# Kernel tuning notes

Hardware: AMD Instinct MI355X
Metric: run time of the kernel (lower is better)

Reference implementation:

```python
import jax, jax.numpy as jnp
import numpy as np

N = 50000
E = 800000
IN_C, HID_C, OUT_C = 128, 256, 128
BN_EPS = 1e-5


def glorot(key, shape):
    fan_in, fan_out = shape
    lim = float(np.sqrt(6.0 / (fan_in + fan_out)))
    return jax.random.uniform(key, shape, jnp.float32, -lim, lim)


def setup_inputs() -> dict:
    key = jax.random.key(0)
    ks = jax.random.split(key, 16)
    inp = {
        "x": jax.random.normal(ks[0], (N, IN_C), jnp.float32),
        "edge_index": jax.random.randint(ks[1], (2, E), 0, N, jnp.int64),
        # SAGEConv 1 (in->hid): lin_l has bias, lin_r has no bias (PyG default)
        "wl1": glorot(ks[2], (IN_C, HID_C)), "bl1": jnp.zeros((HID_C,), jnp.float32),
        "wr1": glorot(ks[3], (IN_C, HID_C)),
        # SAGEConv 2 (hid->hid)
        "wl2": glorot(ks[4], (HID_C, HID_C)), "bl2": jnp.zeros((HID_C,), jnp.float32),
        "wr2": glorot(ks[5], (HID_C, HID_C)),
        # SAGEConv 3 (hid->out)
        "wl3": glorot(ks[6], (HID_C, OUT_C)), "bl3": jnp.zeros((OUT_C,), jnp.float32),
        "wr3": glorot(ks[7], (HID_C, OUT_C)),
        # BatchNorm params (eval mode: running stats)
        "bn1_w": jnp.ones((HID_C,), jnp.float32), "bn1_b": jnp.zeros((HID_C,), jnp.float32),
        "bn1_m": jax.random.normal(ks[8], (HID_C,), jnp.float32) * 0.1,
        "bn1_v": jax.random.uniform(ks[9], (HID_C,), jnp.float32, 0.5, 1.5),
        "bn2_w": jnp.ones((HID_C,), jnp.float32), "bn2_b": jnp.zeros((HID_C,), jnp.float32),
        "bn2_m": jax.random.normal(ks[10], (HID_C,), jnp.float32) * 0.1,
        "bn2_v": jax.random.uniform(ks[11], (HID_C,), jnp.float32, 0.5, 1.5),
    }
    return inp


def sage_conv(x, src, dst, wl, bl, wr):
    # mean aggregation of source-node features at destination nodes
    agg = jax.ops.segment_sum(x[src], dst, num_segments=N)          # [N, d_in]
    deg = jax.ops.segment_sum(jnp.ones((E,), x.dtype), dst, num_segments=N)
    mean = agg / jnp.maximum(deg, 1.0)[:, None]
    return mean @ wl + bl + x @ wr                                   # [N, d_out]


def batch_norm(x, w, b, m, v):
    return (x - m) * jax.lax.rsqrt(v + BN_EPS) * w + b


def reference(x, edge_index, wl1, bl1, wr1, wl2, bl2, wr2, wl3, bl3, wr3,
              bn1_w, bn1_b, bn1_m, bn1_v, bn2_w, bn2_b, bn2_m, bn2_v):
    src, dst = edge_index[0], edge_index[1]
    # layer 1: SAGEConv -> BN -> ReLU (dropout is identity in eval mode)
    h = sage_conv(x, src, dst, wl1, bl1, wr1)
    h = jax.nn.relu(batch_norm(h, bn1_w, bn1_b, bn1_m, bn1_v))
    # layer 2
    h = sage_conv(h, src, dst, wl2, bl2, wr2)
    h = jax.nn.relu(batch_norm(h, bn2_w, bn2_b, bn2_m, bn2_v))
    # output layer: plain SAGEConv
    return sage_conv(h, src, dst, wl3, bl3, wr3)
```

## Files before the change

kernel.cpp:

```cpp
#include <hip/hip_runtime.h>
#include <hip/hip_bf16.h>

#define NN 50000
#define NE 800000
#define NSB 49
#define AGG_BLOCKS 2048

typedef __attribute__((ext_vector_type(8))) short bh8;
typedef __attribute__((ext_vector_type(4))) float f32x4;

static __device__ __forceinline__ unsigned short f2bf(float f){
  unsigned u = __float_as_uint(f);
  unsigned r = (u + 0x7fffu + ((u >> 16) & 1u)) >> 16;
  return (unsigned short)r;
}
static __device__ __forceinline__ float bflo(unsigned u){ return __uint_as_float(u << 16); }
static __device__ __forceinline__ float bfhi(unsigned u){ return __uint_as_float(u & 0xffff0000u); }
static __device__ __forceinline__ unsigned packbf2(float lo, float hi){
  return ((unsigned)f2bf(hi) << 16) | (unsigned)f2bf(lo);
}
static __device__ __forceinline__ unsigned char f2fp8(float v){
  return (unsigned char)(__builtin_amdgcn_cvt_pk_fp8_f32(v, v, 0, false) & 0xff);
}

static __device__ __forceinline__ void gload16(const void* g, void* l){
  __builtin_amdgcn_global_load_lds(
      (const __attribute__((address_space(1))) unsigned int*)g,
      (__attribute__((address_space(3))) unsigned int*)l, 16, 0, 0);
}

__global__ void hist_k(const int* __restrict__ dstv, int* __restrict__ cnt,
                       int* __restrict__ rank){
  int i = blockIdx.x * 256 + threadIdx.x;
  if (i < NE) rank[i] = atomicAdd(&cnt[dstv[i]], 1);
}

__global__ __launch_bounds__(256) void scan1_k(const int* __restrict__ cnt,
                                               int* __restrict__ rowp,
                                               int* __restrict__ bsum){
  __shared__ int sa[256], sb[256];
  const int t = threadIdx.x, blk = blockIdx.x;
  const int base = blk * 1024 + t * 4;
  int4 v = make_int4(0, 0, 0, 0);
  if (base + 3 < NN) v = *reinterpret_cast<const int4*>(cnt + base);
  else if (base < NN){
    v.x = cnt[base];
    if (base + 1 < NN) v.y = cnt[base + 1];
    if (base + 2 < NN) v.z = cnt[base + 2];
  }
  const int s = v.x + v.y + v.z + v.w;
  sa[t] = s; __syncthreads();
  int* a = sa; int* b = sb;
  for (int off = 1; off < 256; off <<= 1){
    int val = a[t]; if (t >= off) val += a[t - off];
    b[t] = val; __syncthreads();
    int* tmp = a; a = b; b = tmp;
  }
  const int ex = a[t] - s;
  if (base < NN){
    rowp[base] = ex;
    if (base + 1 < NN) rowp[base + 1] = ex + v.x;
    if (base + 2 < NN) rowp[base + 2] = ex + v.x + v.y;
    if (base + 3 < NN) rowp[base + 3] = ex + v.x + v.y + v.z;
  }
  if (t == 255) bsum[blk] = a[255];
}

__global__ void scan2_k(int* __restrict__ bsum){
  __shared__ int s[64];
  const int t = threadIdx.x;
  s[t] = (t < NSB) ? bsum[t] : 0;
  __syncthreads();
  if (t == 0){
    int run = 0;
    for (int i = 0; i < NSB; ++i){ int c = s[i]; s[i] = run; run += c; }
  }
  __syncthreads();
  if (t < NSB) bsum[t] = s[t];
}

__global__ __launch_bounds__(256) void scan3_k(int* __restrict__ rowp,
                                               const int* __restrict__ bsum){
  const int blk = blockIdx.x;
  const int base = blk * 1024 + threadIdx.x * 4;
  const int off = bsum[blk];
  #pragma unroll
  for (int i = 0; i < 4; ++i){
    int idx = base + i;
    if (idx < NN) rowp[idx] += off;
  }
  if (blk == 0 && threadIdx.x == 0) rowp[NN] = NE;
}

__global__ __launch_bounds__(256) void fill_k(const int* __restrict__ srcv,
                       const int* __restrict__ dstv,
                       const int* __restrict__ rank,
                       const int* __restrict__ rowp, int* __restrict__ csrc){
  const int part  = blockIdx.x & 7;
  const int chunk = blockIdx.x >> 3;
  const int lo = part * (NN / 8);
  const int hi = lo + (NN / 8);
  const int base = chunk * (NE / 128);
  const int endi = base + (NE / 128);
  for (int i = base + threadIdx.x; i < endi; i += 256){
    int d = dstv[i];
    if (d >= lo && d < hi){
      csrc[rowp[d] + rank[i]] = srcv[i];
    }
  }
}

__global__ void f2b_k(const float4* __restrict__ x, uint2* __restrict__ xb,
                      unsigned* __restrict__ xq){
  int i = blockIdx.x * 256 + threadIdx.x;
  if (i < NN * 128 / 4){
    float4 v = x[i];
    uint2 o; o.x = packbf2(v.x, v.y); o.y = packbf2(v.z, v.w);
    xb[i] = o;
    int w = 0;
    w = __builtin_amdgcn_cvt_pk_fp8_f32(v.x, v.y, w, false);
    w = __builtin_amdgcn_cvt_pk_fp8_f32(v.z, v.w, w, true);
    xq[i] = (unsigned)w;
  }
}

__global__ void prep_k(const float* __restrict__ wl1, const float* __restrict__ wr1,
                       const float* __restrict__ wl2, const float* __restrict__ wr2,
                       const float* __restrict__ wl3, const float* __restrict__ wr3,
                       const float* __restrict__ bl1, const float* __restrict__ bl2,
                       const float* __restrict__ bn1w, const float* __restrict__ bn1b,
                       const float* __restrict__ bn1m, const float* __restrict__ bn1v,
                       const float* __restrict__ bn2w, const float* __restrict__ bn2b,
                       const float* __restrict__ bn2m, const float* __restrict__ bn2v,
                       unsigned short* __restrict__ B1t, unsigned short* __restrict__ B2t,
                       unsigned short* __restrict__ B3t,
                       float* __restrict__ S1, float* __restrict__ T1,
                       float* __restrict__ S2, float* __restrict__ T2){
  int i = blockIdx.x * 256 + threadIdx.x;
  if (i < 65536){
    int n = i >> 8, k = i & 255;
    float v = (k < 128) ? wl1[k * 256 + n] : wr1[(k - 128) * 256 + n];
    B1t[n * 256 + k] = f2bf(v);
  } else if (i < 65536 + 131072){
    int j = i - 65536; int n = j >> 9, k = j & 511;
    float v = (k < 256) ? wl2[k * 256 + n] : wr2[(k - 256) * 256 + n];
    B2t[n * 512 + k] = f2bf(v);
  } else if (i < 65536 + 131072 + 65536){
    int j = i - (65536 + 131072); int n = j >> 8, k = j & 255;
    float v = (n < 128) ? wl3[k * 128 + n] : wr3[k * 128 + (n - 128)];
    B3t[n * 256 + k] = f2bf(v);
  } else if (i < 65536 + 131072 + 65536 + 512){
    int j = i - (65536 + 131072 + 65536);
    if (j < 256){
      float s = bn1w[j] * rsqrtf(bn1v[j] + 1e-5f);
      S1[j] = s; T1[j] = (bl1[j] - bn1m[j]) * s + bn1b[j];
    } else {
      int c = j - 256;
      float s = bn2w[c] * rsqrtf(bn2v[c] + 1e-5f);
      S2[c] = s; T2[c] = (bl2[c] - bn2m[c]) * s + bn2b[c];
    }
  }
}

__global__ __launch_bounds__(256) void agg128q_k(const unsigned short* __restrict__ featq,
                         unsigned* __restrict__ out,
                         const int* __restrict__ rowp, const int* __restrict__ csrc){
  const int lane = threadIdx.x & 63;
  const int node0 = __builtin_amdgcn_readfirstlane(blockIdx.x * 4 + (threadIdx.x >> 6));
  const int nw = gridDim.x * 4;
  for (int node = node0; node < NN; node += nw){
    const int start = rowp[node], end = rowp[node + 1];
    float a0 = 0.f, a1 = 0.f, b0 = 0.f, b1 = 0.f;
    int e = start;
    for (; e + 7 < end; e += 8){
      unsigned u0 = featq[(size_t)csrc[e]     * 64 + lane];
      unsigned u1 = featq[(size_t)csrc[e + 1] * 64 + lane];
      unsigned u2 = featq[(size_t)csrc[e + 2] * 64 + lane];
      unsigned u3 = featq[(size_t)csrc[e + 3] * 64 + lane];
      unsigned u4 = featq[(size_t)csrc[e + 4] * 64 + lane];
      unsigned u5 = featq[(size_t)csrc[e + 5] * 64 + lane];
      unsigned u6 = featq[(size_t)csrc[e + 6] * 64 + lane];
      unsigned u7 = featq[(size_t)csrc[e + 7] * 64 + lane];
      a0 += __builtin_amdgcn_cvt_f32_fp8(u0, 0); a1 += __builtin_amdgcn_cvt_f32_fp8(u0, 1);
      b0 += __builtin_amdgcn_cvt_f32_fp8(u1, 0); b1 += __builtin_amdgcn_cvt_f32_fp8(u1, 1);
      a0 += __builtin_amdgcn_cvt_f32_fp8(u2, 0); a1 += __builtin_amdgcn_cvt_f32_fp8(u2, 1);
      b0 += __builtin_amdgcn_cvt_f32_fp8(u3, 0); b1 += __builtin_amdgcn_cvt_f32_fp8(u3, 1);
      a0 += __builtin_amdgcn_cvt_f32_fp8(u4, 0); a1 += __builtin_amdgcn_cvt_f32_fp8(u4, 1);
      b0 += __builtin_amdgcn_cvt_f32_fp8(u5, 0); b1 += __builtin_amdgcn_cvt_f32_fp8(u5, 1);
      a0 += __builtin_amdgcn_cvt_f32_fp8(u6, 0); a1 += __builtin_amdgcn_cvt_f32_fp8(u6, 1);
      b0 += __builtin_amdgcn_cvt_f32_fp8(u7, 0); b1 += __builtin_amdgcn_cvt_f32_fp8(u7, 1);
    }
    for (; e < end; ++e){
      unsigned u = featq[(size_t)csrc[e] * 64 + lane];
      a0 += __builtin_amdgcn_cvt_f32_fp8(u, 0); a1 += __builtin_amdgcn_cvt_f32_fp8(u, 1);
    }
    int d = end - start;
    float inv = 1.f / (float)(d > 0 ? d : 1);
    out[(size_t)node * 64 + lane] = packbf2((a0 + b0) * inv, (a1 + b1) * inv);
  }
}

#define DEC8(u, x0, x1, x2, x3) { \
  x0 += __builtin_amdgcn_cvt_f32_fp8((u), 0); \
  x1 += __builtin_amdgcn_cvt_f32_fp8((u), 1); \
  x2 += __builtin_amdgcn_cvt_f32_fp8((u), 2); \
  x3 += __builtin_amdgcn_cvt_f32_fp8((u), 3); }

__global__ __launch_bounds__(256) void agg256q_k(const unsigned* __restrict__ featq, unsigned* __restrict__ out,
                         const int* __restrict__ rowp, const int* __restrict__ csrc){
  const int lane = threadIdx.x & 63;
  const int node0 = __builtin_amdgcn_readfirstlane(blockIdx.x * 4 + (threadIdx.x >> 6));
  const int nw = gridDim.x * 4;
  for (int node = node0; node < NN; node += nw){
    const int start = rowp[node], end = rowp[node + 1];
    float a0 = 0.f, a1 = 0.f, a2 = 0.f, a3 = 0.f;
    float b0 = 0.f, b1 = 0.f, b2 = 0.f, b3 = 0.f;
    int e = start;
    for (; e + 7 < end; e += 8){
      unsigned u0 = featq[(size_t)csrc[e]     * 64 + lane];
      unsigned u1 = featq[(size_t)csrc[e + 1] * 64 + lane];
      unsigned u2 = featq[(size_t)csrc[e + 2] * 64 + lane];
      unsigned u3 = featq[(size_t)csrc[e + 3] * 64 + lane];
      unsigned u4 = featq[(size_t)csrc[e + 4] * 64 + lane];
      unsigned u5 = featq[(size_t)csrc[e + 5] * 64 + lane];
      unsigned u6 = featq[(size_t)csrc[e + 6] * 64 + lane];
      unsigned u7 = featq[(size_t)csrc[e + 7] * 64 + lane];
      DEC8(u0, a0, a1, a2, a3) DEC8(u1, b0, b1, b2, b3)
      DEC8(u2, a0, a1, a2, a3) DEC8(u3, b0, b1, b2, b3)
      DEC8(u4, a0, a1, a2, a3) DEC8(u5, b0, b1, b2, b3)
      DEC8(u6, a0, a1, a2, a3) DEC8(u7, b0, b1, b2, b3)
    }
    for (; e < end; ++e){
      unsigned u = featq[(size_t)csrc[e] * 64 + lane];
      DEC8(u, a0, a1, a2, a3)
    }
    int d = end - start;
    float inv = 1.f / (float)(d > 0 ? d : 1);
    uint2 o; o.x = packbf2((a0 + b0) * inv, (a1 + b1) * inv);
    o.y = packbf2((a2 + b2) * inv, (a3 + b3) * inv);
    *reinterpret_cast<uint2*>(out + (size_t)node * 128 + lane * 2) = o;
  }
}

__global__ __launch_bounds__(256) void final_k(const unsigned short* __restrict__ tq, float* __restrict__ out,
                        const int* __restrict__ rowp, const int* __restrict__ csrc,
                        const float* __restrict__ bl3){
  const int lane = threadIdx.x & 63;
  const int node0 = __builtin_amdgcn_readfirstlane(blockIdx.x * 4 + (threadIdx.x >> 6));
  const int nw = gridDim.x * 4;
  for (int node = node0; node < NN; node += nw){
    const int start = rowp[node], end = rowp[node + 1];
    float a0 = 0.f, a1 = 0.f, b0 = 0.f, b1 = 0.f;
    int e = start;
    for (; e + 7 < end; e += 8){
      unsigned u0 = tq[(size_t)csrc[e]     * 64 + lane];
      unsigned u1 = tq[(size_t)csrc[e + 1] * 64 + lane];
      unsigned u2 = tq[(size_t)csrc[e + 2] * 64 + lane];
      unsigned u3 = tq[(size_t)csrc[e + 3] * 64 + lane];
      unsigned u4 = tq[(size_t)csrc[e + 4] * 64 + lane];
      unsigned u5 = tq[(size_t)csrc[e + 5] * 64 + lane];
      unsigned u6 = tq[(size_t)csrc[e + 6] * 64 + lane];
      unsigned u7 = tq[(size_t)csrc[e + 7] * 64 + lane];
      a0 += __builtin_amdgcn_cvt_f32_fp8(u0, 0); a1 += __builtin_amdgcn_cvt_f32_fp8(u0, 1);
      b0 += __builtin_amdgcn_cvt_f32_fp8(u1, 0); b1 += __builtin_amdgcn_cvt_f32_fp8(u1, 1);
      a0 += __builtin_amdgcn_cvt_f32_fp8(u2, 0); a1 += __builtin_amdgcn_cvt_f32_fp8(u2, 1);
      b0 += __builtin_amdgcn_cvt_f32_fp8(u3, 0); b1 += __builtin_amdgcn_cvt_f32_fp8(u3, 1);
      a0 += __builtin_amdgcn_cvt_f32_fp8(u4, 0); a1 += __builtin_amdgcn_cvt_f32_fp8(u4, 1);
      b0 += __builtin_amdgcn_cvt_f32_fp8(u5, 0); b1 += __builtin_amdgcn_cvt_f32_fp8(u5, 1);
      a0 += __builtin_amdgcn_cvt_f32_fp8(u6, 0); a1 += __builtin_amdgcn_cvt_f32_fp8(u6, 1);
      b0 += __builtin_amdgcn_cvt_f32_fp8(u7, 0); b1 += __builtin_amdgcn_cvt_f32_fp8(u7, 1);
    }
    for (; e < end; ++e){
      unsigned u = tq[(size_t)csrc[e] * 64 + lane];
      a0 += __builtin_amdgcn_cvt_f32_fp8(u, 0); a1 += __builtin_amdgcn_cvt_f32_fp8(u, 1);
    }
    int d = end - start;
    float inv = 1.f / (float)(d > 0 ? d : 1);
    float2* o = reinterpret_cast<float2*>(out + (size_t)node * 128) + lane;
    float2 v = *o;
    v.x += (a0 + b0) * inv + bl3[lane * 2];
    v.y += (a1 + b1) * inv + bl3[lane * 2 + 1];
    *o = v;
  }
}

template<int KTOT, int K0, int MODE>
__global__ __launch_bounds__(256) void gemm_k(
    const unsigned short* __restrict__ A0, const unsigned short* __restrict__ A1,
    const unsigned short* __restrict__ Bt,
    const float* __restrict__ S, const float* __restrict__ Tt,
    unsigned short* __restrict__ outB, unsigned char* __restrict__ outQ,
    float* __restrict__ outF, int M)
{
  __shared__ __align__(16) unsigned char lds[49152];
  const int tid = threadIdx.x;
  const int lane = tid & 63;
  const int wv = tid >> 6;
  const int wm = wv >> 1, wn = wv & 1;

  const int nwg = gridDim.x;
  const int q = nwg >> 3, r8 = nwg & 7;
  const int xcd = blockIdx.x & 7, idx = blockIdx.x >> 3;
  const int wg = (xcd < r8) ? xcd * (q + 1) + idx : r8 * (q + 1) + (xcd - r8) * q + idx;
  const int bm = wg >> 1, bn = wg & 1;

  const int rr0 = tid >> 2,         g0 = (tid & 3) ^ ((tid >> 3) & 3);
  const int rr1 = (tid + 256) >> 2, g1 = ((tid + 256) & 3) ^ (((tid + 256) >> 3) & 3);
  int growA0 = bm * 128 + rr0; if (growA0 > M - 1) growA0 = M - 1;
  int growA1 = bm * 128 + rr1; if (growA1 > M - 1) growA1 = M - 1;
  const size_t browA0 = (size_t)(bn * 128 + rr0) * KTOT;
  const size_t browA1 = (size_t)(bn * 128 + rr1) * KTOT;

  const int l15 = lane & 15, kg = lane >> 4;
  const int slot = (kg ^ ((l15 >> 1) & 3)) * 16;

  constexpr int NT = KTOT / 32;

  auto STAGE = [&](int buf, int kt){
    const int kb = kt * 32;
    const unsigned short* Ap; int pitch, kk;
    if (KTOT == K0 || kb < K0){ Ap = A0; pitch = K0; kk = kb; }
    else { Ap = A1; pitch = KTOT - K0; kk = kb - K0; }
    unsigned char* base = lds + buf * 16384;
    gload16(Ap + (size_t)growA0 * pitch + kk + g0 * 8, base + tid * 16);
    gload16(Ap + (size_t)growA1 * pitch + kk + g1 * 8, base + 4096 + tid * 16);
    gload16(Bt + browA0 + kb + g0 * 8, base + 8192 + tid * 16);
    gload16(Bt + browA1 + kb + g1 * 8, base + 12288 + tid * 16);
  };

  f32x4 acc[4][4];
  #pragma unroll
  for (int i = 0; i < 4; ++i)
    #pragma unroll
    for (int j = 0; j < 4; ++j){ acc[i][j][0]=0.f; acc[i][j][1]=0.f; acc[i][j][2]=0.f; acc[i][j][3]=0.f; }

  STAGE(0, 0);
  if (NT > 1) STAGE(1, 1);

  int rb = 0, sb = 2;
  for (int kt = 0; kt < NT; ++kt){
    if (kt < NT - 1) asm volatile("s_waitcnt vmcnt(4)" ::: "memory");
    else             asm volatile("s_waitcnt vmcnt(0)" ::: "memory");
    __builtin_amdgcn_s_barrier();
    __builtin_amdgcn_sched_barrier(0);

    if (kt + 2 < NT){ STAGE(sb, kt + 2); sb = (sb == 2) ? 0 : sb + 1; }

    unsigned char* base = lds + rb * 16384;
    rb = (rb == 2) ? 0 : rb + 1;

    bh8 af[4], bf[4];
    #pragma unroll
    for (int mi = 0; mi < 4; ++mi){
      int rA = wm * 64 + mi * 16 + l15;
      af[mi] = *reinterpret_cast<const bh8*>(base + rA * 64 + slot);
    }
    #pragma unroll
    for (int ni = 0; ni < 4; ++ni){
      int rB = wn * 64 + ni * 16 + l15;
      bf[ni] = *reinterpret_cast<const bh8*>(base + 8192 + rB * 64 + slot);
    }
    __builtin_amdgcn_s_setprio(1);
    #pragma unroll
    for (int mi = 0; mi < 4; ++mi)
      #pragma unroll
      for (int ni = 0; ni < 4; ++ni)
        acc[mi][ni] = __builtin_amdgcn_mfma_f32_16x16x32_bf16(af[mi], bf[ni], acc[mi][ni], 0, 0, 0);
    __builtin_amdgcn_s_setprio(0);
  }

  #pragma unroll
  for (int mi = 0; mi < 4; ++mi){
    int rbase = bm * 128 + wm * 64 + mi * 16 + ((lane >> 4) << 2);
    #pragma unroll
    for (int ni = 0; ni < 4; ++ni){
      int col = bn * 128 + wn * 64 + ni * 16 + (lane & 15);
      #pragma unroll
      for (int j = 0; j < 4; ++j){
        int row = rbase + j;
        if (row < M){
          float v = acc[mi][ni][j];
          if (MODE == 0){
            v = v * S[col] + Tt[col];
            v = v > 0.f ? v : 0.f;
            outB[(size_t)row * 256 + col] = f2bf(v);
            if (outQ) outQ[(size_t)row * 256 + col] = f2fp8(v);
          } else {
            if (col < 128) outQ[(size_t)row * 128 + col] = f2fp8(v);
            else           outF[(size_t)row * 128 + (col - 128)] = v;
          }
        }
      }
    }
  }
}

extern "C" void kernel_launch(void* const* d_in, const int* in_sizes, int n_in,
                              void* d_out, int out_size, void* d_ws, size_t ws_size,
                              hipStream_t stream) {
  (void)in_sizes; (void)n_in; (void)out_size; (void)ws_size;
  const float* x   = (const float*)d_in[0];
  const int*   ei  = (const int*)d_in[1];
  const int*   srcv = ei;
  const int*   dstv = ei + NE;
  const float* wl1 = (const float*)d_in[2];
  const float* bl1 = (const float*)d_in[3];
  const float* wr1 = (const float*)d_in[4];
  const float* wl2 = (const float*)d_in[5];
  const float* bl2 = (const float*)d_in[6];
  const float* wr2 = (const float*)d_in[7];
  const float* wl3 = (const float*)d_in[8];
  const float* bl3 = (const float*)d_in[9];
  const float* wr3 = (const float*)d_in[10];
  const float* bn1w = (const float*)d_in[11];
  const float* bn1b = (const float*)d_in[12];
  const float* bn1m = (const float*)d_in[13];
  const float* bn1v = (const float*)d_in[14];
  const float* bn2w = (const float*)d_in[15];
  const float* bn2b = (const float*)d_in[16];
  const float* bn2m = (const float*)d_in[17];
  const float* bn2v = (const float*)d_in[18];

  char* ws = (char*)d_ws;
  size_t off = 0;
  auto alloc = [&](size_t bytes) -> void* {
    void* p = ws + off;
    off += (bytes + 255) & ~(size_t)255;
    return p;
  };
  int* cnt  = (int*)alloc((size_t)NN * 4);
  int* rank = (int*)alloc((size_t)NE * 4);
  int* rowp = (int*)alloc((size_t)(NN + 1) * 4);
  int* csrc = (int*)alloc((size_t)NE * 4);
  int* bsum = (int*)alloc((size_t)NSB * 4);
  unsigned short* B1t = (unsigned short*)alloc(256 * 256 * 2);
  unsigned short* B2t = (unsigned short*)alloc(256 * 512 * 2);
  unsigned short* B3t = (unsigned short*)alloc(256 * 256 * 2);
  float* S1 = (float*)alloc(256 * 4);
  float* T1 = (float*)alloc(256 * 4);
  float* S2 = (float*)alloc(256 * 4);
  float* T2 = (float*)alloc(256 * 4);
  unsigned short* xb   = (unsigned short*)alloc((size_t)NN * 128 * 2);
  unsigned short* agg1 = (unsigned short*)alloc((size_t)NN * 128 * 2);
  unsigned short* h1   = (unsigned short*)alloc((size_t)NN * 256 * 2);
  unsigned short* h2   = (unsigned short*)alloc((size_t)NN * 256 * 2);
  unsigned short* agg2 = xb;
  unsigned char*  h1q  = (unsigned char*)h2;
  unsigned*       xq   = (unsigned*)((unsigned char*)h2 + (size_t)NN * 256);
  unsigned char*  tq   = (unsigned char*)h1;
  float* outp = (float*)d_out;

  hipMemsetAsync(cnt, 0, (size_t)NN * 4, stream);
  hist_k<<<(NE + 255) / 256, 256, 0, stream>>>(dstv, cnt, rank);
  scan1_k<<<NSB, 256, 0, stream>>>(cnt, rowp, bsum);
  scan2_k<<<1, 64, 0, stream>>>(bsum);
  scan3_k<<<NSB, 256, 0, stream>>>(rowp, bsum);
  fill_k<<<1024, 256, 0, stream>>>(srcv, dstv, rank, rowp, csrc);
  prep_k<<<1026, 256, 0, stream>>>(wl1, wr1, wl2, wr2, wl3, wr3, bl1, bl2,
                                   bn1w, bn1b, bn1m, bn1v, bn2w, bn2b, bn2m, bn2v,
                                   B1t, B2t, B3t, S1, T1, S2, T2);
  f2b_k<<<(NN * 128 / 4 + 255) / 256, 256, 0, stream>>>((const float4*)x, (uint2*)xb, xq);

  agg128q_k<<<AGG_BLOCKS, 256, 0, stream>>>((const unsigned short*)xq, (unsigned*)agg1, rowp, csrc);
  gemm_k<256, 128, 0><<<782, 256, 0, stream>>>(agg1, xb, B1t, S1, T1, h1, h1q, nullptr, NN);
  agg256q_k<<<AGG_BLOCKS, 256, 0, stream>>>((const unsigned*)h1q, (unsigned*)agg2, rowp, csrc);
  gemm_k<512, 256, 0><<<782, 256, 0, stream>>>(agg2, h1, B2t, S2, T2, h2, nullptr, nullptr, NN);
  gemm_k<256, 256, 1><<<782, 256, 0, stream>>>(h2, h2, B3t, nullptr, nullptr, nullptr, tq, outp, NN);
  final_k<<<AGG_BLOCKS, 256, 0, stream>>>((const unsigned short*)tq, outp, rowp, csrc, bl3);
}
```

Baseline: 252.3 us.

## Restructure GEMM into barrier-free per-wave private tiles with smaller blocks

Each GEMM workgroup now has two waves. Each wave owns a private double-buffered LDS region and loads its own A and B tiles, so the block-wide s_barrier is gone. The block tile shrinks from 128x256 to 64x256, which doubles the grid, and each wave duplicates the A-tile loads its partner also makes. This removes cross-wave synchronisation stalls and lowers LDS per block for higher occupancy, at the cost of redundant global and LDS traffic for A and one less pipeline stage.

```diff
diff --git a/kernel.cpp b/kernel.cpp
--- a/kernel.cpp
+++ b/kernel.cpp
@@ -285,34 +285,36 @@
 }
 
 template<int KTOT, int K0, int MODE>
-__global__ __launch_bounds__(256) void gemm_k(
+__global__ __launch_bounds__(128) void gemm_k(
     const unsigned short* __restrict__ A0, const unsigned short* __restrict__ A1,
     const unsigned short* __restrict__ Bt,
     const float* __restrict__ S, const float* __restrict__ Tt,
     unsigned short* __restrict__ outB, unsigned char* __restrict__ outQ,
     float* __restrict__ outF, int M)
 {
-  __shared__ __align__(16) unsigned char lds[49152];
+  __shared__ __align__(16) unsigned char lds[32768];
   const int tid = threadIdx.x;
   const int lane = tid & 63;
   const int wv = tid >> 6;
-  const int wm = wv >> 1, wn = wv & 1;
-
   const int nwg = gridDim.x;
   const int q = nwg >> 3, r8 = nwg & 7;
   const int xcd = blockIdx.x & 7, idx = blockIdx.x >> 3;
   const int wg = (xcd < r8) ? xcd * (q + 1) + idx : r8 * (q + 1) + (xcd - r8) * q + idx;
   const int bm = wg >> 1, bn = wg & 1;
 
-  const int rr0 = tid >> 2,         g0 = (tid & 3) ^ ((tid >> 3) & 3);
-  const int rr1 = (tid + 256) >> 2, g1 = ((tid + 256) & 3) ^ (((tid + 256) >> 3) & 3);
-  int growA0 = bm * 128 + rr0; if (growA0 > M - 1) growA0 = M - 1;
-  int growA1 = bm * 128 + rr1; if (growA1 > M - 1) growA1 = M - 1;
-  const size_t browA0 = (size_t)(bn * 128 + rr0) * KTOT;
-  const size_t browA1 = (size_t)(bn * 128 + rr1) * KTOT;
-
   const int l15 = lane & 15, kg = lane >> 4;
   const int slot = (kg ^ ((l15 >> 1) & 3)) * 16;
+  const int g   = (lane & 3) ^ ((lane >> 3) & 3);
+  const int r16 = lane >> 2;
+
+  const int ncol0 = bn * 128 + wv * 64;
+  int arow[4];
+  #pragma unroll
+  for (int i = 0; i < 4; ++i){
+    int r = bm * 64 + i * 16 + r16;
+    arow[i] = (r > M - 1) ? (M - 1) : r;
+  }
+  unsigned char* wbase = lds + wv * 16384;
 
   constexpr int NT = KTOT / 32;
 
@@ -321,11 +323,14 @@
     const unsigned short* Ap; int pitch, kk;
     if (KTOT == K0 || kb < K0){ Ap = A0; pitch = K0; kk = kb; }
     else { Ap = A1; pitch = KTOT - K0; kk = kb - K0; }
-    unsigned char* base = lds + buf * 16384;
-    gload16(Ap + (size_t)growA0 * pitch + kk + g0 * 8, base + tid * 16);
-    gload16(Ap + (size_t)growA1 * pitch + kk + g1 * 8, base + 4096 + tid * 16);
-    gload16(Bt + browA0 + kb + g0 * 8, base + 8192 + tid * 16);
-    gload16(Bt + browA1 + kb + g1 * 8, base + 12288 + tid * 16);
+    unsigned char* base = wbase + buf * 8192;
+    #pragma unroll
+    for (int i = 0; i < 4; ++i)
+      gload16(Ap + (size_t)arow[i] * pitch + kk + g * 8, base + i * 1024 + lane * 16);
+    #pragma unroll
+    for (int i = 0; i < 4; ++i)
+      gload16(Bt + (size_t)(ncol0 + i * 16 + r16) * KTOT + kb + g * 8,
+              base + 4096 + i * 1024 + lane * 16);
   };
 
   f32x4 acc[4][4];
@@ -337,29 +342,24 @@
   STAGE(0, 0);
   if (NT > 1) STAGE(1, 1);
 
-  int rb = 0, sb = 2;
   for (int kt = 0; kt < NT; ++kt){
-    if (kt < NT - 1) asm volatile("s_waitcnt vmcnt(4)" ::: "memory");
+    if (kt < NT - 1) asm volatile("s_waitcnt vmcnt(8)" ::: "memory");
     else             asm volatile("s_waitcnt vmcnt(0)" ::: "memory");
-    __builtin_amdgcn_s_barrier();
     __builtin_amdgcn_sched_barrier(0);
 
-    if (kt + 2 < NT){ STAGE(sb, kt + 2); sb = (sb == 2) ? 0 : sb + 1; }
-
-    unsigned char* base = lds + rb * 16384;
-    rb = (rb == 2) ? 0 : rb + 1;
-
+    unsigned char* base = wbase + (kt & 1) * 8192;
     bh8 af[4], bf[4];
     #pragma unroll
-    for (int mi = 0; mi < 4; ++mi){
-      int rA = wm * 64 + mi * 16 + l15;
-      af[mi] = *reinterpret_cast<const bh8*>(base + rA * 64 + slot);
-    }
-    #pragma unroll
-    for (int ni = 0; ni < 4; ++ni){
-      int rB = wn * 64 + ni * 16 + l15;
-      bf[ni] = *reinterpret_cast<const bh8*>(base + 8192 + rB * 64 + slot);
-    }
+    for (int mi = 0; mi < 4; ++mi)
+      af[mi] = *reinterpret_cast<const bh8*>(base + (mi * 16 + l15) * 64 + slot);
+    #pragma unroll
+    for (int ni = 0; ni < 4; ++ni)
+      bf[ni] = *reinterpret_cast<const bh8*>(base + 4096 + (ni * 16 + l15) * 64 + slot);
+
+    asm volatile("s_waitcnt lgkmcnt(0)" ::: "memory");
+    __builtin_amdgcn_sched_barrier(0);
+    if (kt + 2 < NT) STAGE(kt & 1, kt + 2);
+
     __builtin_amdgcn_s_setprio(1);
     #pragma unroll
     for (int mi = 0; mi < 4; ++mi)
@@ -371,10 +371,10 @@
 
   #pragma unroll
   for (int mi = 0; mi < 4; ++mi){
-    int rbase = bm * 128 + wm * 64 + mi * 16 + ((lane >> 4) << 2);
+    int rbase = bm * 64 + mi * 16 + (kg << 2);
     #pragma unroll
     for (int ni = 0; ni < 4; ++ni){
-      int col = bn * 128 + wn * 64 + ni * 16 + (lane & 15);
+      int col = ncol0 + ni * 16 + l15;
       #pragma unroll
       for (int j = 0; j < 4; ++j){
         int row = rbase + j;
@@ -462,9 +462,9 @@
   f2b_k<<<(NN * 128 / 4 + 255) / 256, 256, 0, stream>>>((const float4*)x, (uint2*)xb, xq);
 
   agg128q_k<<<AGG_BLOCKS, 256, 0, stream>>>((const unsigned short*)xq, (unsigned*)agg1, rowp, csrc);
-  gemm_k<256, 128, 0><<<782, 256, 0, stream>>>(agg1, xb, B1t, S1, T1, h1, h1q, nullptr, NN);
+  gemm_k<256, 128, 0><<<1564, 128, 0, stream>>>(agg1, xb, B1t, S1, T1, h1, h1q, nullptr, NN);
   agg256q_k<<<AGG_BLOCKS, 256, 0, stream>>>((const unsigned*)h1q, (unsigned*)agg2, rowp, csrc);
-  gemm_k<512, 256, 0><<<782, 256, 0, stream>>>(agg2, h1, B2t, S2, T2, h2, nullptr, nullptr, NN);
-  gemm_k<256, 256, 1><<<782, 256, 0, stream>>>(h2, h2, B3t, nullptr, nullptr, nullptr, tq, outp, NN);
+  gemm_k<512, 256, 0><<<1564, 128, 0, stream>>>(agg2, h1, B2t, S2, T2, h2, nullptr, nullptr, NN);
+  gemm_k<256, 256, 1><<<1564, 128, 0, stream>>>(h2, h2, B3t, nullptr, nullptr, nullptr, tq, outp, NN);
   final_k<<<AGG_BLOCKS, 256, 0, stream>>>((const unsigned short*)tq, outp, rowp, csrc, bl3);
 }
```

Result: slower. 268.3 us (+6.3%).

## Fuse layer-2 GEMM with layer-3 projection GEMM via LDS-resident hidden tile

Applied to the files above, without the earlier changes.

Merges the layer-2 SAGE GEMM (with BN+ReLU epilogue) and the layer-3 projection GEMM into one kernel. The 64x256 bf16 h2 tile stays in LDS, swizzled, and feeds the second MFMA loop directly, so h2 is never written to or re-read from global memory and one launch is removed. The second loop reads B3 straight from global memory with no LDS staging, and the larger LDS footprint plus two accumulator sets may reduce occupancy. tq is moved to alias h2's buffer.

```diff
diff --git a/kernel.cpp b/kernel.cpp
--- a/kernel.cpp
+++ b/kernel.cpp
@@ -395,6 +395,147 @@
   }
 }
 
+__global__ __launch_bounds__(256) void gemm23_k(
+    const unsigned short* __restrict__ A0 ,
+    const unsigned short* __restrict__ A1 ,
+    const unsigned short* __restrict__ B2 ,
+    const unsigned short* __restrict__ B3 ,
+    const float* __restrict__ S, const float* __restrict__ Tt,
+    unsigned char* __restrict__ tq, float* __restrict__ outF, int M)
+{
+  __shared__ __align__(16) unsigned char lds[61440];
+  const int tid = threadIdx.x;
+  const int lane = tid & 63;
+  const int wv = tid >> 6;
+
+  const int nwg = gridDim.x;
+  const int q = nwg >> 3, r8 = nwg & 7;
+  const int xcd = blockIdx.x & 7, idx = blockIdx.x >> 3;
+  const int bm = (xcd < r8) ? xcd * (q + 1) + idx : r8 * (q + 1) + (xcd - r8) * q + idx;
+
+  const int l15 = lane & 15, kg = lane >> 4;
+  const int slot = (kg ^ ((l15 >> 1) & 3)) * 16;
+  const int rr = tid >> 2;
+  const int g  = (tid & 3) ^ ((tid >> 3) & 3);
+  int grow = bm * 64 + rr; if (grow > M - 1) grow = M - 1;
+
+  auto STAGE = [&](int buf, int kt){
+    const int kb = kt * 32;
+    const unsigned short* Ap = (kb < 256) ? A0 : A1;
+    const int kk = (kb < 256) ? kb : kb - 256;
+    unsigned char* base = lds + buf * 20480;
+    gload16(Ap + (size_t)grow * 256 + kk + g * 8, base + tid * 16);
+    gload16(B2 + (size_t)(rr      ) * 512 + kb + g * 8, base +  4096 + tid * 16);
+    gload16(B2 + (size_t)(rr +  64) * 512 + kb + g * 8, base +  8192 + tid * 16);
+    gload16(B2 + (size_t)(rr + 128) * 512 + kb + g * 8, base + 12288 + tid * 16);
+    gload16(B2 + (size_t)(rr + 192) * 512 + kb + g * 8, base + 16384 + tid * 16);
+  };
+
+  f32x4 acc[4][4];
+  #pragma unroll
+  for (int i = 0; i < 4; ++i)
+    #pragma unroll
+    for (int j = 0; j < 4; ++j){ acc[i][j][0]=0.f; acc[i][j][1]=0.f; acc[i][j][2]=0.f; acc[i][j][3]=0.f; }
+
+  STAGE(0, 0);
+  STAGE(1, 1);
+
+  int rb = 0, sb = 2;
+  #pragma unroll 1
+  for (int kt = 0; kt < 16; ++kt){
+    if (kt < 15) asm volatile("s_waitcnt vmcnt(5)" ::: "memory");
+    else         asm volatile("s_waitcnt vmcnt(0)" ::: "memory");
+    __builtin_amdgcn_s_barrier();
+    __builtin_amdgcn_sched_barrier(0);
+
+    if (kt + 2 < 16){ STAGE(sb, kt + 2); sb = (sb == 2) ? 0 : sb + 1; }
+
+    unsigned char* base = lds + rb * 20480;
+    rb = (rb == 2) ? 0 : rb + 1;
+
+    bh8 af[4], bf[4];
+    #pragma unroll
+    for (int mi = 0; mi < 4; ++mi)
+      af[mi] = *reinterpret_cast<const bh8*>(base + (mi * 16 + l15) * 64 + slot);
+    #pragma unroll
+    for (int ni = 0; ni < 4; ++ni)
+      bf[ni] = *reinterpret_cast<const bh8*>(base + 4096 + (wv * 64 + ni * 16 + l15) * 64 + slot);
+
+    __builtin_amdgcn_s_setprio(1);
+    #pragma unroll
+    for (int mi = 0; mi < 4; ++mi)
+      #pragma unroll
+      for (int ni = 0; ni < 4; ++ni)
+        acc[mi][ni] = __builtin_amdgcn_mfma_f32_16x16x32_bf16(bf[ni], af[mi], acc[mi][ni], 0, 0, 0);
+    __builtin_amdgcn_s_setprio(0);
+  }
+
+  __syncthreads();
+  #pragma unroll
+  for (int mi = 0; mi < 4; ++mi){
+    const int row = mi * 16 + l15;
+    #pragma unroll
+    for (int ni = 0; ni < 4; ++ni){
+      const int c0 = wv * 64 + ni * 16 + kg * 4;
+      float v0 = acc[mi][ni][0] * S[c0]     + Tt[c0];     v0 = v0 > 0.f ? v0 : 0.f;
+      float v1 = acc[mi][ni][1] * S[c0 + 1] + Tt[c0 + 1]; v1 = v1 > 0.f ? v1 : 0.f;
+      float v2 = acc[mi][ni][2] * S[c0 + 2] + Tt[c0 + 2]; v2 = v2 > 0.f ? v2 : 0.f;
+      float v3 = acc[mi][ni][3] * S[c0 + 3] + Tt[c0 + 3]; v3 = v3 > 0.f ? v3 : 0.f;
+      uint2 w; w.x = packbf2(v0, v1); w.y = packbf2(v2, v3);
+      const int chunk = wv * 8 + ni * 2 + (kg >> 1);
+      const int byte = row * 512 + ((chunk ^ (row & 7)) * 16) + (kg & 1) * 8;
+      *reinterpret_cast<uint2*>(lds + byte) = w;
+    }
+  }
+  __syncthreads();
+
+  f32x4 acc2[4][4];
+  #pragma unroll
+  for (int i = 0; i < 4; ++i)
+    #pragma unroll
+    for (int j = 0; j < 4; ++j){ acc2[i][j][0]=0.f; acc2[i][j][1]=0.f; acc2[i][j][2]=0.f; acc2[i][j][3]=0.f; }
+
+  #pragma unroll 1
+  for (int kt = 0; kt < 8; ++kt){
+    const int kb = kt * 32;
+    bh8 af2[4], bf2[4];
+    #pragma unroll
+    for (int mi = 0; mi < 4; ++mi){
+      const int row = mi * 16 + l15;
+      const int chunk = kt * 4 + kg;
+      af2[mi] = *reinterpret_cast<const bh8*>(lds + row * 512 + ((chunk ^ (row & 7)) * 16));
+    }
+    #pragma unroll
+    for (int ni = 0; ni < 4; ++ni)
+      bf2[ni] = *reinterpret_cast<const bh8*>(B3 + (size_t)(wv * 64 + ni * 16 + l15) * 256 + kb + kg * 8);
+    __builtin_amdgcn_s_setprio(1);
+    #pragma unroll
+    for (int mi = 0; mi < 4; ++mi)
+      #pragma unroll
+      for (int ni = 0; ni < 4; ++ni)
+        acc2[mi][ni] = __builtin_amdgcn_mfma_f32_16x16x32_bf16(af2[mi], bf2[ni], acc2[mi][ni], 0, 0, 0);
+    __builtin_amdgcn_s_setprio(0);
+  }
+
+  #pragma unroll
+  for (int mi = 0; mi < 4; ++mi){
+    const int rbase = bm * 64 + mi * 16 + (kg << 2);
+    #pragma unroll
+    for (int ni = 0; ni < 4; ++ni){
+      const int col = wv * 64 + ni * 16 + l15;
+      #pragma unroll
+      for (int j = 0; j < 4; ++j){
+        const int row = rbase + j;
+        if (row < M){
+          float v = acc2[mi][ni][j];
+          if (col < 128) tq[(size_t)row * 128 + col] = f2fp8(v);
+          else           outF[(size_t)row * 128 + (col - 128)] = v;
+        }
+      }
+    }
+  }
+}
+
 extern "C" void kernel_launch(void* const* d_in, const int* in_sizes, int n_in,
                               void* d_out, int out_size, void* d_ws, size_t ws_size,
                               hipStream_t stream) {
@@ -447,7 +588,7 @@
   unsigned short* agg2 = xb;
   unsigned char*  h1q  = (unsigned char*)h2;
   unsigned*       xq   = (unsigned*)((unsigned char*)h2 + (size_t)NN * 256);
-  unsigned char*  tq   = (unsigned char*)h1;
+  unsigned char*  tq   = (unsigned char*)h2;
   float* outp = (float*)d_out;
 
   hipMemsetAsync(cnt, 0, (size_t)NN * 4, stream);
@@ -464,7 +605,6 @@
   agg128q_k<<<AGG_BLOCKS, 256, 0, stream>>>((const unsigned short*)xq, (unsigned*)agg1, rowp, csrc);
   gemm_k<256, 128, 0><<<782, 256, 0, stream>>>(agg1, xb, B1t, S1, T1, h1, h1q, nullptr, NN);
   agg256q_k<<<AGG_BLOCKS, 256, 0, stream>>>((const unsigned*)h1q, (unsigned*)agg2, rowp, csrc);
-  gemm_k<512, 256, 0><<<782, 256, 0, stream>>>(agg2, h1, B2t, S2, T2, h2, nullptr, nullptr, NN);
-  gemm_k<256, 256, 1><<<782, 256, 0, stream>>>(h2, h2, B3t, nullptr, nullptr, nullptr, tq, outp, NN);
+  gemm23_k<<<782, 256, 0, stream>>>(agg2, h1, B2t, B3t, S2, T2, tq, outp, NN);
   final_k<<<AGG_BLOCKS, 256, 0, stream>>>((const unsigned short*)tq, outp, rowp, csrc, bl3);
 }
```

Result: faster. 242.0 us (-4.1%).
